# Kernel optimization log

Hardware: AMD Instinct MI355X
Metric: run time of the kernel (lower is better)

## Reference

```python
import jax, jax.numpy as jnp
import numpy as np

EPS = 1e-8
PROB_PENALTY = 1e-4
REV_SCALE = 0.1


def _barycenters(vertices, faces):
    # vertices: [N,3], faces: [F,3] int -> [F,3]
    return vertices[faces].mean(axis=1)


def _pairwise_sq_dists(a, b):
    # a: [P,3], b: [Q,3] -> [P,Q] squared euclidean distances via dot expansion
    a2 = jnp.sum(a * a, axis=-1)  # [P]
    b2 = jnp.sum(b * b, axis=-1)  # [Q]
    return a2[:, None] + b2[None, :] - 2.0 * (a @ b.T)


def setup_inputs() -> dict:
    key = jax.random.key(0)
    k_ov, k_of, k_sv, k_sf, k_fp, k_u1, k_u2 = jax.random.split(key, 7)
    N_ORIG, F_ORIG = 8000, 16000
    N_SIMP, F_SIMP = 2500, 4000
    NUM_SAMPLES = 8
    return {
        "original_vertices": jax.random.normal(k_ov, (N_ORIG, 3), dtype=jnp.float32),
        "original_faces": jax.random.randint(k_of, (F_ORIG, 3), 0, N_ORIG, dtype=jnp.int64) if jax.config.jax_enable_x64 else jax.random.randint(k_of, (F_ORIG, 3), 0, N_ORIG, dtype=jnp.int32),
        "simplified_vertices": jax.random.normal(k_sv, (N_SIMP, 3), dtype=jnp.float32),
        "simplified_faces": jax.random.randint(k_sf, (F_SIMP, 3), 0, N_SIMP, dtype=jnp.int32),
        "face_probabilities": jax.random.uniform(k_fp, (F_SIMP,), dtype=jnp.float32),
        "u1": jax.random.uniform(k_u1, (F_SIMP, NUM_SAMPLES, 1), dtype=jnp.float32),
        "u2": jax.random.uniform(k_u2, (F_SIMP, NUM_SAMPLES, 1), dtype=jnp.float32),
    }


def reference(original_vertices, original_faces, simplified_vertices,
              simplified_faces, face_probabilities, u1, u2):
    num_samples = u1.shape[1]

    # ---- forward term: simplified barycenters -> nearest original barycenter ----
    simp_bc = _barycenters(simplified_vertices, simplified_faces)  # [Fs,3]
    orig_bc = _barycenters(original_vertices, original_faces)      # [Fo,3]
    min_d2 = jnp.min(_pairwise_sq_dists(simp_bc, orig_bc), axis=1)  # [Fs]
    forward_term = jnp.sum(face_probabilities * min_d2) \
        + PROB_PENALTY * jnp.sum(1.0 - face_probabilities)

    # ---- reverse term: sample points on simplified triangles, 1-NN to original verts ----
    fv = simplified_vertices[simplified_faces]  # [Fs,3(verts),3(xyz)]
    r1 = jnp.sqrt(u1)                           # [Fs,S,1]
    a = 1.0 - r1
    b = r1 * (1.0 - u2)
    c = r1 * u2
    samples = (a * fv[:, None, 0] + b * fv[:, None, 1] + c * fv[:, None, 2])  # [Fs,S,3]
    pts = samples.reshape(-1, 3)  # [Fs*S,3]

    # brute-force 1-NN squared distances (pytorch3d knn convention)
    min_dist = jnp.min(_pairwise_sq_dists(pts, original_vertices), axis=1)  # [Fs*S]
    scaled = (min_dist / (jnp.max(min_dist) + EPS)) * REV_SCALE
    fp_expanded = jnp.repeat(face_probabilities, num_samples)  # [Fs*S]
    reverse_term = jnp.sum(fp_expanded * scaled)

    return forward_term + reverse_term
```

## Files before the change

kernel.cpp:

```cpp
#include <hip/hip_runtime.h>

#define EPSF 1e-8f
#define PROB_PENALTYF 1e-4f
#define REV_SCALEF 0.1f
#define INFBITS 0x7F800000u
#define ONEBF ((unsigned short)0x3F80)
#define SENT_C 1.0e6f

#define PTW 8
#define WPB 4
#define FBLK 256

typedef __attribute__((ext_vector_type(8))) short short8;
typedef __attribute__((ext_vector_type(4))) float f32x4;

__device__ __forceinline__ unsigned short bfh(float f) {
    unsigned u = __float_as_uint(f);
    return (unsigned short)((u + 0x7FFFu + ((u >> 16) & 1u)) >> 16);
}
__device__ __forceinline__ float bftof(unsigned short h) {
    return __uint_as_float(((unsigned)h) << 16);
}
__device__ __forceinline__ unsigned short bfl(float f, unsigned short h) {
    return bfh(f - bftof(h));
}
__device__ __forceinline__ unsigned pk(unsigned short lo, unsigned short hi) {
    return (unsigned)lo | ((unsigned)hi << 16);
}

__device__ __forceinline__ uint4 makeAfrag(float x, float y, float z, float w, int g) {
    unsigned short hx = bfh(x), hy = bfh(y), hz = bfh(z);
    uint4 r;
    if (g == 0) {
        unsigned short lx = bfl(x, hx), ly = bfl(y, hy), lz = bfl(z, hz);
        r.x = pk(hx, hy); r.y = pk(hz, lx); r.z = pk(ly, lz); r.w = pk(hx, hy);
    } else {
        unsigned short hw = bfh(w), lw = bfl(w, hw);
        r.x = pk(hz, ONEBF); r.y = pk(ONEBF, hw); r.z = pk(lw, 0); r.w = 0u;
    }
    return r;
}
__device__ __forceinline__ uint4 makeBfrag(float x, float y, float z, float w, int g) {
    unsigned short hx = bfh(x), hy = bfh(y), hz = bfh(z);
    uint4 r;
    if (g == 0) {
        unsigned short lx = bfl(x, hx), ly = bfl(y, hy);
        r.x = pk(hx, hy); r.y = pk(hz, hx); r.z = pk(hy, hz); r.w = pk(lx, ly);
    } else {
        unsigned short lz = bfl(z, hz);
        unsigned short hw = bfh(w), lw = bfl(w, hw);
        r.x = pk(lz, hw); r.y = pk(lw, ONEBF); r.z = pk(ONEBF, 0); r.w = 0u;
    }
    return r;
}

__global__ void prep_kernel(const float* __restrict__ overts,
                            const int* __restrict__ ofaces,
                            const float* __restrict__ sverts,
                            const int* __restrict__ sfaces,
                            const float* __restrict__ u1,
                            const float* __restrict__ u2,
                            uint4* __restrict__ revA, uint4* __restrict__ fwdA,
                            uint4* __restrict__ revB, uint4* __restrict__ fwdB,
                            unsigned* __restrict__ rev_min,
                            unsigned* __restrict__ fwd_min,
                            float* __restrict__ acc,
                            int n_orig, int f_orig, int fs, int S, int npts,
                            int revPt, int fwdPt, int revSt, int fwdSt) {
    int tid = blockIdx.x * blockDim.x + threadIdx.x;
    const float third = 1.0f / 3.0f;
    int r0 = revPt * 32, r1 = r0 + fwdPt * 32, r2 = r1 + revSt * 32, r3 = r2 + fwdSt * 32;

    if (tid < r0) {
        int l = tid & 31, g = l >> 4;
        int k = (tid >> 5) * 16 + (l & 15);
        float x = 0.f, y = 0.f, z = 0.f;
        if (k < npts) {
            int f = k / S;
            float rr = sqrtf(u1[k]);
            float uu = u2[k];
            float wa = 1.0f - rr, wb = rr * (1.0f - uu), wc = rr * uu;
            int a = sfaces[3 * f], b = sfaces[3 * f + 1], c = sfaces[3 * f + 2];
            x = wa * sverts[3 * a] + wb * sverts[3 * b] + wc * sverts[3 * c];
            y = wa * sverts[3 * a + 1] + wb * sverts[3 * b + 1] + wc * sverts[3 * c + 1];
            z = wa * sverts[3 * a + 2] + wb * sverts[3 * b + 2] + wc * sverts[3 * c + 2];
        }
        float p2 = x * x + y * y + z * z;
        revA[tid] = makeAfrag(-2.f * x, -2.f * y, -2.f * z, p2, g);
    } else if (tid < r1) {
        int t2 = tid - r0;
        int l = t2 & 31, g = l >> 4;
        int k = (t2 >> 5) * 16 + (l & 15);
        float x = 0.f, y = 0.f, z = 0.f;
        if (k < fs) {
            int a = sfaces[3 * k], b = sfaces[3 * k + 1], c = sfaces[3 * k + 2];
            x = (sverts[3 * a] + sverts[3 * b] + sverts[3 * c]) * third;
            y = (sverts[3 * a + 1] + sverts[3 * b + 1] + sverts[3 * c + 1]) * third;
            z = (sverts[3 * a + 2] + sverts[3 * b + 2] + sverts[3 * c + 2]) * third;
        }
        float p2 = x * x + y * y + z * z;
        fwdA[t2] = makeAfrag(-2.f * x, -2.f * y, -2.f * z, p2, g);
    } else if (tid < r2) {
        int t2 = tid - r1;
        int l = t2 & 31, g = l >> 4;
        int s = (t2 >> 5) * 16 + (l & 15);
        float x = SENT_C, y = SENT_C, z = SENT_C;
        if (s < n_orig) { x = overts[3 * s]; y = overts[3 * s + 1]; z = overts[3 * s + 2]; }
        revB[t2] = makeBfrag(x, y, z, x * x + y * y + z * z, g);
    } else if (tid < r3) {
        int t2 = tid - r2;
        int l = t2 & 31, g = l >> 4;
        int s = (t2 >> 5) * 16 + (l & 15);
        float x = SENT_C, y = SENT_C, z = SENT_C;
        if (s < f_orig) {
            int a = ofaces[3 * s], b = ofaces[3 * s + 1], c = ofaces[3 * s + 2];
            x = (overts[3 * a] + overts[3 * b] + overts[3 * c]) * third;
            y = (overts[3 * a + 1] + overts[3 * b + 1] + overts[3 * c + 1]) * third;
            z = (overts[3 * a + 2] + overts[3 * b + 2] + overts[3 * c + 2]) * third;
        }
        fwdB[t2] = makeBfrag(x, y, z, x * x + y * y + z * z, g);
    } else {
        int t2 = tid - r3;
        if (t2 < npts) rev_min[t2] = INFBITS;
        if (t2 < fs)   fwd_min[t2] = INFBITS;
        if (t2 < 8)    acc[t2] = 0.0f;
    }
}

__global__ void __launch_bounds__(256, 2)
mfma_min_kernel(const uint4* __restrict__ revA, const uint4* __restrict__ fwdA,
                const uint4* __restrict__ revB, const uint4* __restrict__ fwdB,
                unsigned* __restrict__ rev_min, unsigned* __restrict__ fwd_min,
                int revGroups, int revWaves, int revPt, int revNpts, int revSt, int revCS,
                int fwdGroups, int fwdPt, int fwdNpts, int fwdSt, int fwdCS,
                int totalWaves) {
    int gw = blockIdx.x * WPB + ((int)threadIdx.x >> 6);
    if (gw >= totalWaves) return;
    int lane = (int)threadIdx.x & 63;

    const uint4 *A, *B;
    unsigned* omin;
    int group, chunk, cs, nTile, npts, nst;
    if (gw < revWaves) {
        A = revA; B = revB; omin = rev_min; nTile = revPt; npts = revNpts; nst = revSt;
        cs = revCS; group = gw % revGroups; chunk = gw / revGroups;
    } else {
        int g2 = gw - revWaves;
        A = fwdA; B = fwdB; omin = fwd_min; nTile = fwdPt; npts = fwdNpts; nst = fwdSt;
        cs = fwdCS; group = g2 % fwdGroups; chunk = g2 / fwdGroups;
    }
    int s0 = chunk * cs;
    int ns = min(cs, nst - s0);

    const short8* A8 = reinterpret_cast<const short8*>(A);
    const short8* B8 = reinterpret_cast<const short8*>(B);

    const short8 zero8 = {0, 0, 0, 0, 0, 0, 0, 0};
    short8 a[PTW];
    int pt0 = group * PTW;
    #pragma unroll
    for (int r = 0; r < PTW; ++r) {
        int ptile = min(pt0 + r, nTile - 1);
        short8 av = A8[ptile * 32 + (lane & 31)];
        a[r] = (lane < 32) ? av : zero8;
    }

    float inf = __uint_as_float(INFBITS);
    f32x4 m[PTW];
    #pragma unroll
    for (int r = 0; r < PTW; ++r) m[r] = (f32x4){inf, inf, inf, inf};
    f32x4 cz = {0.f, 0.f, 0.f, 0.f};
    const short8* bp = B8 + (size_t)s0 * 32 + (lane & 31);

#define COMPUTE(BB)                                                              \
    do {                                                                         \
        _Pragma("unroll")                                                        \
        for (int r = 0; r < PTW; ++r) {                                          \
            f32x4 d = __builtin_amdgcn_mfma_f32_16x16x32_bf16(a[r], (BB), cz, 0, 0, 0); \
            m[r].x = fminf(m[r].x, d.x); m[r].y = fminf(m[r].y, d.y);            \
            m[r].z = fminf(m[r].z, d.z); m[r].w = fminf(m[r].w, d.w);            \
        }                                                                        \
    } while (0)

    short8 b0 = bp[0];
    short8 b1 = bp[32];
    int s = 0;
    for (; s + 2 <= ns; s += 2) {
        short8 n0 = bp[(s + 2) * 32];
        short8 n1 = bp[(s + 3) * 32];
        COMPUTE(b0);
        COMPUTE(b1);
        b0 = n0; b1 = n1;
    }
    if (s < ns) COMPUTE(b0);
#undef COMPUTE

    #pragma unroll
    for (int off = 1; off < 16; off <<= 1) {
        #pragma unroll
        for (int r = 0; r < PTW; ++r) {
            m[r].x = fminf(m[r].x, __shfl_xor(m[r].x, off));
            m[r].y = fminf(m[r].y, __shfl_xor(m[r].y, off));
            m[r].z = fminf(m[r].z, __shfl_xor(m[r].z, off));
            m[r].w = fminf(m[r].w, __shfl_xor(m[r].w, off));
        }
    }

    if ((lane & 15) == 0) {
        int rowbase = (lane >> 4) * 4;
        #pragma unroll
        for (int r = 0; r < PTW; ++r) {
            int pb = min(pt0 + r, nTile - 1) * 16 + rowbase;
            if (pb + 0 < npts) atomicMin(&omin[pb + 0], __float_as_uint(fmaxf(m[r].x, 0.f)));
            if (pb + 1 < npts) atomicMin(&omin[pb + 1], __float_as_uint(fmaxf(m[r].y, 0.f)));
            if (pb + 2 < npts) atomicMin(&omin[pb + 2], __float_as_uint(fmaxf(m[r].z, 0.f)));
            if (pb + 3 < npts) atomicMin(&omin[pb + 3], __float_as_uint(fmaxf(m[r].w, 0.f)));
        }
    }
}

__global__ void finalize_kernel(const unsigned int* __restrict__ fwd_min,
                                const unsigned int* __restrict__ rev_min,
                                const float* __restrict__ fp,
                                float* acc, float* out,
                                int fs, int npts, int S, int nblocks) {
    __shared__ float s1[FBLK], s2[FBLK], s3[FBLK];
    int k = blockIdx.x * blockDim.x + threadIdx.x;
    float fsum = 0.f, rsum = 0.f, rmax = 0.f;
    if (k < npts) {
        float md = __uint_as_float(rev_min[k]);
        float p = fp[k / S];
        rsum = p * md;
        rmax = md;
    }
    if (k < fs) {
        float p = fp[k];
        fsum = p * __uint_as_float(fwd_min[k]) + PROB_PENALTYF * (1.0f - p);
    }
    s1[threadIdx.x] = fsum;
    s2[threadIdx.x] = rsum;
    s3[threadIdx.x] = rmax;
    __syncthreads();
    for (int off = FBLK / 2; off > 0; off >>= 1) {
        if ((int)threadIdx.x < off) {
            s1[threadIdx.x] += s1[threadIdx.x + off];
            s2[threadIdx.x] += s2[threadIdx.x + off];
            s3[threadIdx.x] = fmaxf(s3[threadIdx.x], s3[threadIdx.x + off]);
        }
        __syncthreads();
    }
    if (threadIdx.x == 0) {
        atomicAdd(&acc[0], s1[0]);
        atomicAdd(&acc[1], s2[0]);
        atomicMax((unsigned int*)&acc[2], __float_as_uint(s3[0]));
        __threadfence();
        unsigned int ticket = atomicAdd((unsigned int*)&acc[3], 1u);
        if (ticket == (unsigned int)(nblocks - 1)) {
            __threadfence();
            float a0 = atomicAdd(&acc[0], 0.0f);
            float a1 = atomicAdd(&acc[1], 0.0f);
            unsigned int mb = atomicOr((unsigned int*)&acc[2], 0u);
            out[0] = a0 + a1 * (REV_SCALEF / (__uint_as_float(mb) + EPSF));
        }
    }
}

extern "C" void kernel_launch(void* const* d_in, const int* in_sizes, int n_in,
                              void* d_out, int out_size, void* d_ws, size_t ws_size,
                              hipStream_t stream) {
    const float* overts = (const float*)d_in[0];
    const int*   ofaces = (const int*)d_in[1];
    const float* sverts = (const float*)d_in[2];
    const int*   sfaces = (const int*)d_in[3];
    const float* fp     = (const float*)d_in[4];
    const float* u1     = (const float*)d_in[5];
    const float* u2     = (const float*)d_in[6];
    float* out = (float*)d_out;

    const int N_ORIG = in_sizes[0] / 3;
    const int F_ORIG = in_sizes[1] / 3;
    const int F_SIMP = in_sizes[3] / 3;
    const int S      = in_sizes[5] / F_SIMP;
    const int NPTS   = F_SIMP * S;

    const int revPt = (NPTS + 15) / 16;
    const int fwdPt = (F_SIMP + 15) / 16;
    const int revSt = (N_ORIG + 15) / 16;
    const int fwdSt = (F_ORIG + 15) / 16;

    uint4* revA = (uint4*)d_ws;
    uint4* fwdA = revA + (size_t)revPt * 32;
    uint4* revB = fwdA + (size_t)fwdPt * 32;
    uint4* fwdB = revB + (size_t)revSt * 32;
    unsigned* rev_min = (unsigned*)(fwdB + (size_t)fwdSt * 32);
    unsigned* fwd_min = rev_min + NPTS;
    float* acc = (float*)(fwd_min + F_SIMP);

    int prepThreads = (revPt + fwdPt + revSt + fwdSt) * 32 + NPTS;
    hipLaunchKernelGGL(prep_kernel, dim3((prepThreads + 255) / 256), dim3(256), 0, stream,
                       overts, ofaces, sverts, sfaces, u1, u2,
                       revA, fwdA, revB, fwdB, rev_min, fwd_min, acc,
                       N_ORIG, F_ORIG, F_SIMP, S, NPTS,
                       revPt, fwdPt, revSt, fwdSt);

    const int revGroups = (revPt + PTW - 1) / PTW;
    const int revChunks = 8;
    const int revCS = (revSt + revChunks - 1) / revChunks;
    const int revWaves = revGroups * revChunks;

    const int fwdGroups = (fwdPt + PTW - 1) / PTW;
    const int fwdChunks = 16;
    const int fwdCS = (fwdSt + fwdChunks - 1) / fwdChunks;
    const int fwdWaves = fwdGroups * fwdChunks;

    const int totalWaves = revWaves + fwdWaves;
    const int mblocks = (totalWaves + WPB - 1) / WPB;
    hipLaunchKernelGGL(mfma_min_kernel, dim3(mblocks), dim3(256), 0, stream,
                       revA, fwdA, revB, fwdB, rev_min, fwd_min,
                       revGroups, revWaves, revPt, NPTS, revSt, revCS,
                       fwdGroups, fwdPt, F_SIMP, fwdSt, fwdCS,
                       totalWaves);

    const int finBlocks = (NPTS + FBLK - 1) / FBLK;
    hipLaunchKernelGGL(finalize_kernel, dim3(finBlocks), dim3(FBLK), 0, stream,
                       fwd_min, rev_min, fp, acc, out, F_SIMP, NPTS, S, finBlocks);
}
```

Measured before the change: 46.69 us.

## Stage B tiles in shared LDS double buffer across block waves, shrink point tiles

Each block's four waves now cooperatively load B-operand tiles into a double-buffered shared-memory array and all read them from there, instead of every wave streaming B from global memory independently. Point tiles per wave drop from 8 to 4, with a fixed chunk size of 64 tiles and launch bounds raised for higher occupancy. Groups are padded to a multiple of four so each block's waves share one chunk. The cost is a block-wide barrier per group of 8 tiles and more redundant MFMA setup per wave.

```diff
diff --git a/kernel.cpp b/kernel.cpp
--- a/kernel.cpp
+++ b/kernel.cpp
@@ -7,12 +7,18 @@
 #define ONEBF ((unsigned short)0x3F80)
 #define SENT_C 1.0e6f
 
-#define PTW 8
+#define PTW 4
 #define WPB 4
+#define CS 64
+#define NG 8
 #define FBLK 256
 
 typedef __attribute__((ext_vector_type(8))) short short8;
 typedef __attribute__((ext_vector_type(4))) float f32x4;
+
+__device__ __forceinline__ float min3f(float a, float b, float c) {
+    return fminf(fminf(a, b), c);
+}
 
 __device__ __forceinline__ unsigned short bfh(float f) {
     unsigned u = __float_as_uint(f);
@@ -127,30 +133,29 @@
     }
 }
 
-__global__ void __launch_bounds__(256, 2)
+__global__ void __launch_bounds__(256, 4)
 mfma_min_kernel(const uint4* __restrict__ revA, const uint4* __restrict__ fwdA,
                 const uint4* __restrict__ revB, const uint4* __restrict__ fwdB,
                 unsigned* __restrict__ rev_min, unsigned* __restrict__ fwd_min,
-                int revGroups, int revWaves, int revPt, int revNpts, int revSt, int revCS,
-                int fwdGroups, int fwdPt, int fwdNpts, int fwdSt, int fwdCS,
-                int totalWaves) {
-    int gw = blockIdx.x * WPB + ((int)threadIdx.x >> 6);
-    if (gw >= totalWaves) return;
-    int lane = (int)threadIdx.x & 63;
+                int revGroups, int revWaves, int revPt, int revNpts, int revSt,
+                int fwdGroups, int fwdPt, int fwdNpts, int fwdSt) {
+    __shared__ short8 lds[2][NG * 32];
+    int tid = (int)threadIdx.x;
+    int gw = blockIdx.x * WPB + (tid >> 6);
+    int lane = tid & 63;
 
     const uint4 *A, *B;
     unsigned* omin;
-    int group, chunk, cs, nTile, npts, nst;
+    int group, chunk, nTile, npts, nst;
     if (gw < revWaves) {
         A = revA; B = revB; omin = rev_min; nTile = revPt; npts = revNpts; nst = revSt;
-        cs = revCS; group = gw % revGroups; chunk = gw / revGroups;
+        group = gw % revGroups; chunk = gw / revGroups;
     } else {
         int g2 = gw - revWaves;
         A = fwdA; B = fwdB; omin = fwd_min; nTile = fwdPt; npts = fwdNpts; nst = fwdSt;
-        cs = fwdCS; group = g2 % fwdGroups; chunk = g2 / fwdGroups;
-    }
-    int s0 = chunk * cs;
-    int ns = min(cs, nst - s0);
+        group = g2 % fwdGroups; chunk = g2 / fwdGroups;
+    }
+    int s0 = chunk * CS;
 
     const short8* A8 = reinterpret_cast<const short8*>(A);
     const short8* B8 = reinterpret_cast<const short8*>(B);
@@ -161,7 +166,7 @@
     #pragma unroll
     for (int r = 0; r < PTW; ++r) {
         int ptile = min(pt0 + r, nTile - 1);
-        short8 av = A8[ptile * 32 + (lane & 31)];
+        short8 av = A8[(size_t)ptile * 32 + (lane & 31)];
         a[r] = (lane < 32) ? av : zero8;
     }
 
@@ -170,30 +175,40 @@
     #pragma unroll
     for (int r = 0; r < PTW; ++r) m[r] = (f32x4){inf, inf, inf, inf};
     f32x4 cz = {0.f, 0.f, 0.f, 0.f};
-    const short8* bp = B8 + (size_t)s0 * 32 + (lane & 31);
-
-#define COMPUTE(BB)                                                              \
-    do {                                                                         \
-        _Pragma("unroll")                                                        \
-        for (int r = 0; r < PTW; ++r) {                                          \
-            f32x4 d = __builtin_amdgcn_mfma_f32_16x16x32_bf16(a[r], (BB), cz, 0, 0, 0); \
-            m[r].x = fminf(m[r].x, d.x); m[r].y = fminf(m[r].y, d.y);            \
-            m[r].z = fminf(m[r].z, d.z); m[r].w = fminf(m[r].w, d.w);            \
-        }                                                                        \
-    } while (0)
-
-    short8 b0 = bp[0];
-    short8 b1 = bp[32];
-    int s = 0;
-    for (; s + 2 <= ns; s += 2) {
-        short8 n0 = bp[(s + 2) * 32];
-        short8 n1 = bp[(s + 3) * 32];
-        COMPUTE(b0);
-        COMPUTE(b1);
-        b0 = n0; b1 = n1;
-    }
-    if (s < ns) COMPUTE(b0);
-#undef COMPUTE
+
+    {
+        int gtile = min(s0 + (tid >> 5), nst - 1);
+        lds[0][tid] = B8[(size_t)gtile * 32 + (tid & 31)];
+    }
+    __syncthreads();
+
+    int cur = 0;
+    for (int g = 0; g < NG; ++g) {
+        short8 vn;
+        if (g + 1 < NG) {
+            int gtile = min(s0 + (g + 1) * 8 + (tid >> 5), nst - 1);
+            vn = B8[(size_t)gtile * 32 + (tid & 31)];
+        }
+        #pragma unroll
+        for (int lt = 0; lt < 8; lt += 2) {
+            short8 b0 = lds[cur][lt * 32 + (lane & 31)];
+            short8 b1 = lds[cur][(lt + 1) * 32 + (lane & 31)];
+            #pragma unroll
+            for (int r = 0; r < PTW; ++r) {
+                f32x4 d0 = __builtin_amdgcn_mfma_f32_16x16x32_bf16(a[r], b0, cz, 0, 0, 0);
+                f32x4 d1 = __builtin_amdgcn_mfma_f32_16x16x32_bf16(a[r], b1, cz, 0, 0, 0);
+                m[r].x = min3f(m[r].x, d0.x, d1.x);
+                m[r].y = min3f(m[r].y, d0.y, d1.y);
+                m[r].z = min3f(m[r].z, d0.z, d1.z);
+                m[r].w = min3f(m[r].w, d0.w, d1.w);
+            }
+        }
+        if (g + 1 < NG) {
+            lds[cur ^ 1][tid] = vn;
+        }
+        __syncthreads();
+        cur ^= 1;
+    }
 
     #pragma unroll
     for (int off = 1; off < 16; off <<= 1) {
@@ -303,23 +318,20 @@
                        N_ORIG, F_ORIG, F_SIMP, S, NPTS,
                        revPt, fwdPt, revSt, fwdSt);
 
-    const int revGroups = (revPt + PTW - 1) / PTW;
-    const int revChunks = 8;
-    const int revCS = (revSt + revChunks - 1) / revChunks;
+    const int revGroups = (((revPt + PTW - 1) / PTW + 3) & ~3);
+    const int revChunks = (revSt + CS - 1) / CS;
     const int revWaves = revGroups * revChunks;
 
-    const int fwdGroups = (fwdPt + PTW - 1) / PTW;
-    const int fwdChunks = 16;
-    const int fwdCS = (fwdSt + fwdChunks - 1) / fwdChunks;
+    const int fwdGroups = (((fwdPt + PTW - 1) / PTW + 3) & ~3);
+    const int fwdChunks = (fwdSt + CS - 1) / CS;
     const int fwdWaves = fwdGroups * fwdChunks;
 
     const int totalWaves = revWaves + fwdWaves;
-    const int mblocks = (totalWaves + WPB - 1) / WPB;
+    const int mblocks = totalWaves / WPB;
     hipLaunchKernelGGL(mfma_min_kernel, dim3(mblocks), dim3(256), 0, stream,
                        revA, fwdA, revB, fwdB, rev_min, fwd_min,
-                       revGroups, revWaves, revPt, NPTS, revSt, revCS,
-                       fwdGroups, fwdPt, F_SIMP, fwdSt, fwdCS,
-                       totalWaves);
+                       revGroups, revWaves, revPt, NPTS, revSt,
+                       fwdGroups, fwdPt, F_SIMP, fwdSt);
 
     const int finBlocks = (NPTS + FBLK - 1) / FBLK;
     hipLaunchKernelGGL(finalize_kernel, dim3(finBlocks), dim3(FBLK), 0, stream,
```

Measured after the change: 40.76 us. -12.7%, faster.
